# Kernel tuning notes

Measured on AMD Instinct MI355X. Metric: run time of the kernel, lower is better.

## Reference

```python
import jax, jax.numpy as jnp
import numpy as np

B, S, N, C, D = 1, 6, 6400, 128, 4
HEADS, POINTS = 4, 20
HS, WS = 32, 88
M = HS * WS
DH = C // HEADS


def setup_inputs() -> dict:
    key = jax.random.key(0)
    ks = jax.random.split(key, 16)
    sc = 0.02
    return {
        "query": jax.random.normal(ks[0], (B, N, C), jnp.float32),
        "key": jax.random.normal(ks[1], (S, M, B, C), jnp.float32),
        "value": jax.random.normal(ks[2], (S, M, B, C), jnp.float32),
        "query_pos": jax.random.normal(ks[3], (B, N, C), jnp.float32),
        "reference_points_cam": jax.random.uniform(ks[4], (S, B, N, D, 2), jnp.float32),
        "bev_mask": jax.random.bernoulli(ks[5], 0.3, (S, B, N, D)),
        "spatial_shapes": jnp.array([[HS, WS]], jnp.int32),
        "level_start_index": jnp.zeros((1,), jnp.int32),
        "Wv": sc * jax.random.normal(ks[6], (C, C), jnp.float32),
        "bv": jnp.zeros((C,), jnp.float32),
        "Woff": sc * jax.random.normal(ks[7], (C, HEADS * POINTS * 2), jnp.float32),
        "boff": sc * jax.random.normal(ks[8], (HEADS * POINTS * 2,), jnp.float32),
        "Wattn": sc * jax.random.normal(ks[9], (C, HEADS * POINTS), jnp.float32),
        "battn": jnp.zeros((HEADS * POINTS,), jnp.float32),
        "Wout": sc * jax.random.normal(ks[10], (C, C), jnp.float32),
        "bout": jnp.zeros((C,), jnp.float32),
    }


def _bilinear(img, x, y):
    # img: (G, HS, WS, DH); x, y: (G, Q, P) pixel coords (grid_sample align_corners=False, zero padding)
    G = img.shape[0]
    flat = img.reshape(G, HS * WS, DH)
    x0 = jnp.floor(x)
    y0 = jnp.floor(y)
    wx1 = x - x0
    wy1 = y - y0
    x0i = x0.astype(jnp.int32)
    y0i = y0.astype(jnp.int32)

    def gather(xi, yi):
        valid = ((xi >= 0) & (xi < WS) & (yi >= 0) & (yi < HS)).astype(img.dtype)
        idx = jnp.clip(yi, 0, HS - 1) * WS + jnp.clip(xi, 0, WS - 1)
        v = jnp.take_along_axis(flat, idx.reshape(G, -1, 1), axis=1)
        return v.reshape(*idx.shape, DH) * valid[..., None]

    v00 = gather(x0i, y0i)
    v01 = gather(x0i + 1, y0i)
    v10 = gather(x0i, y0i + 1)
    v11 = gather(x0i + 1, y0i + 1)
    return (v00 * ((1 - wx1) * (1 - wy1))[..., None]
            + v01 * (wx1 * (1 - wy1))[..., None]
            + v10 * ((1 - wx1) * wy1)[..., None]
            + v11 * (wx1 * wy1)[..., None])


def _deform_attn(q, v, ref, spatial_shapes, Wv, bv, Woff, boff, Wattn, battn):
    # q: (bs, nq, C); v: (bs, M, C); ref: (bs, nq, D, 2) in [0,1]
    bs, nq, _ = q.shape
    val = (v @ Wv + bv).reshape(bs, HS, WS, HEADS, DH)
    val = val.transpose(0, 3, 1, 2, 4).reshape(bs * HEADS, HS, WS, DH)
    # sampling offsets, normalized by (W, H), split points into POINTS//D groups per Z-anchor
    norm = jnp.stack([spatial_shapes[0, 1], spatial_shapes[0, 0]]).astype(q.dtype)  # [W, H]
    off = (q @ Woff + boff).reshape(bs, nq, HEADS, POINTS // D, D, 2) / norm
    loc = ref[:, :, None, None, :, :] + off  # (bs, nq, HEADS, P//D, D, 2)
    loc = loc.reshape(bs, nq, HEADS, POINTS, 2).transpose(0, 2, 1, 3, 4)
    loc = loc.reshape(bs * HEADS, nq, POINTS, 2)
    x = loc[..., 0] * WS - 0.5
    y = loc[..., 1] * HS - 0.5
    sampled = _bilinear(val, x, y)  # (bs*HEADS, nq, POINTS, DH)
    aw = jax.nn.softmax((q @ Wattn + battn).reshape(bs, nq, HEADS, POINTS), axis=-1)
    aw = aw.transpose(0, 2, 1, 3).reshape(bs * HEADS, nq, POINTS)
    out = jnp.einsum('gnpd,gnp->gnd', sampled, aw)
    return out.reshape(bs, HEADS, nq, DH).transpose(0, 2, 1, 3).reshape(bs, nq, C)


def reference(query, key, value, query_pos, reference_points_cam, bev_mask,
              spatial_shapes, level_start_index,
              Wv, bv, Woff, boff, Wattn, battn, Wout, bout):
    residual = query
    q = query + query_pos
    # camera routing mask (original derives indexes from batch 0 of bev_mask)
    mask0 = (bev_mask[:, 0].sum(-1) > 0).astype(q.dtype)  # (S, N)
    # dense masked equivalent of gather/pad/attend/scatter-add: deformable attn is
    # per-query independent, so computing all queries per camera and masking is exact.
    qs = jnp.broadcast_to(q[:, None], (B, S, N, C)).reshape(B * S, N, C)
    vs = value.transpose(2, 0, 1, 3).reshape(B * S, M, C)
    refs = reference_points_cam.transpose(1, 0, 2, 3, 4).reshape(B * S, N, D, 2)
    out = _deform_attn(qs, vs, refs, spatial_shapes, Wv, bv, Woff, boff, Wattn, battn)
    out = out.reshape(B, S, N, C)
    slots = (out * mask0[None, :, :, None]).sum(1)  # (B, N, C)
    count = (bev_mask.sum(-1) > 0).astype(q.dtype).transpose(1, 2, 0).sum(-1)  # (B, N)
    slots = slots / jnp.maximum(count, 1.0)[..., None]
    slots = slots @ Wout + bout
    return slots + residual  # dropout is identity in eval
```

## Files before the change

kernel.cpp:

```cpp
#include <hip/hip_runtime.h>

#define SC 6
#define NQ 6400
#define CH 128
#define HSY 32
#define WSX 88
#define MV 2816
#define NH 4
#define NP 20
#define DD 4
#define DHC 32
#define NPG 5
#define NPAIR (SC * NH * NP)

#define NB_QPROJ 800
#define NB_VPROJ 1056
#define NB_MEGA  (1 + NB_QPROJ + NB_VPROJ)

#define WS_QOFF     38464
#define WS_AW       1062464
#define WS_VAL      1574464
#define WS_SLOTS    3737152

__device__ __forceinline__ unsigned short f32_to_bf16(float x) {
    unsigned int u = __float_as_uint(x);
    unsigned int r = (u + 0x7FFFu + ((u >> 16) & 1u)) >> 16;
    return (unsigned short)r;
}

#define QB 8
__global__ __launch_bounds__(256) void k_mega(
        const unsigned int* __restrict__ bm,
        const float* __restrict__ q, const float* __restrict__ qpos,
        const float* __restrict__ Woff, const float* __restrict__ boff,
        const float* __restrict__ Wattn, const float* __restrict__ battn,
        const float* __restrict__ value, const float* __restrict__ Wv,
        const float* __restrict__ bv,
        int* __restrict__ flag, float* __restrict__ qoff,
        float* __restrict__ aw, unsigned short* __restrict__ valw) {
    __shared__ __align__(16) float smem[2048];
    int bid = blockIdx.x;
    int t = threadIdx.x;

    if (bid == 0) {
        unsigned int* r_or = (unsigned int*)smem;
        unsigned int* r_vi = r_or + 256;
        unsigned int o = 0u, v = 0u;
        for (int i = t; i < 2048; i += 256) {
            unsigned int w = bm[i];
            o |= (w & 0xFFFFFF00u);
            v |= (unsigned int)((w != 0u) & (w != 0x3F800000u));
        }
        r_or[t] = o; r_vi[t] = v;
        __syncthreads();
        for (int s = 128; s > 0; s >>= 1) {
            if (t < s) { r_or[t] |= r_or[t + s]; r_vi[t] |= r_vi[t + s]; }
            __syncthreads();
        }
        if (t == 0) {
            int f;
            if (!r_vi[0]) f = 2;
            else if (r_or[0]) f = 1;
            else f = 0;
            *flag = f;
        }
        return;
    }

    if (bid <= NB_QPROJ) {
        float (*qs)[QB] = (float(*)[QB])smem;
        float (*lg)[NH * NP] = (float(*)[NH * NP])(smem + CH * QB);
        int n0 = (bid - 1) * QB;
        for (int i = t; i < QB * CH; i += 256) {
            int qi = i >> 7, k = i & 127;
            int gi = (n0 + qi) * CH + k;
            qs[k][qi] = q[gi] + qpos[gi];
        }
        __syncthreads();
        if (t < 160) {
            float acc[QB];
#pragma unroll
            for (int qi = 0; qi < QB; ++qi) acc[qi] = 0.f;
            for (int k = 0; k < CH; ++k) {
                float w = Woff[k * 160 + t];
                float4 a = *(const float4*)&qs[k][0];
                float4 b = *(const float4*)&qs[k][4];
                acc[0] += a.x * w; acc[1] += a.y * w; acc[2] += a.z * w; acc[3] += a.w * w;
                acc[4] += b.x * w; acc[5] += b.y * w; acc[6] += b.z * w; acc[7] += b.w * w;
            }
            float b = boff[t];
#pragma unroll
            for (int qi = 0; qi < QB; ++qi) qoff[(n0 + qi) * 160 + t] = acc[qi] + b;
        } else if (t < 240) {
            int j = t - 160;
            float acc[QB];
#pragma unroll
            for (int qi = 0; qi < QB; ++qi) acc[qi] = 0.f;
            for (int k = 0; k < CH; ++k) {
                float w = Wattn[k * 80 + j];
                float4 a = *(const float4*)&qs[k][0];
                float4 b = *(const float4*)&qs[k][4];
                acc[0] += a.x * w; acc[1] += a.y * w; acc[2] += a.z * w; acc[3] += a.w * w;
                acc[4] += b.x * w; acc[5] += b.y * w; acc[6] += b.z * w; acc[7] += b.w * w;
            }
            float b = battn[j];
#pragma unroll
            for (int qi = 0; qi < QB; ++qi) lg[qi][j] = acc[qi] + b;
        }
        __syncthreads();
        if (t < QB * NH) {
            int qi = t >> 2, h = t & 3;
            float mx = -1e30f;
#pragma unroll
            for (int p = 0; p < NP; ++p) mx = fmaxf(mx, lg[qi][h * NP + p]);
            float e[NP];
            float sm = 0.f;
#pragma unroll
            for (int p = 0; p < NP; ++p) { e[p] = __expf(lg[qi][h * NP + p] - mx); sm += e[p]; }
            float inv = 1.f / sm;
#pragma unroll
            for (int p = 0; p < NP; ++p) aw[(n0 + qi) * 80 + h * NP + p] = e[p] * inv;
        }
        return;
    }

    {
        float (*vs)[16] = (float(*)[16])smem;
        int r0 = (bid - 1 - NB_QPROJ) * 16;
        for (int i = t; i < 16 * CH; i += 256) {
            int ri = i >> 7, k = i & 127;
            vs[k][ri] = value[(size_t)(r0 + ri) * CH + k];
        }
        __syncthreads();
        int c = t & 127, rh = t >> 7;
        float acc[8];
#pragma unroll
        for (int ri = 0; ri < 8; ++ri) acc[ri] = 0.f;
        for (int k = 0; k < CH; ++k) {
            float w = Wv[k * CH + c];
            float4 a = *(const float4*)&vs[k][rh * 8];
            float4 b = *(const float4*)&vs[k][rh * 8 + 4];
            acc[0] += a.x * w; acc[1] += a.y * w; acc[2] += a.z * w; acc[3] += a.w * w;
            acc[4] += b.x * w; acc[5] += b.y * w; acc[6] += b.z * w; acc[7] += b.w * w;
        }
        float b = bv[c];
        int h = c >> 5, dh = c & 31;
#pragma unroll
        for (int ri = 0; ri < 8; ++ri) {
            int r = r0 + rh * 8 + ri;
            int s = r / MV;
            int m = r - s * MV;
            valw[(size_t)((s * NH + h) * MV + m) * DHC + dh] = f32_to_bf16(acc[ri] + b);
        }
    }
}

#define REDP 36
__global__ __launch_bounds__(320) void k_sample(
        const float* __restrict__ ref, const float* __restrict__ qoff,
        const float* __restrict__ aw, const void* __restrict__ bm,
        const int* __restrict__ flag, const unsigned short* __restrict__ valw,
        float* __restrict__ slots) {
    int bid = blockIdx.x;
    int n = (bid & 7) * (NQ / 8) + (bid >> 3);
    int t = threadIdx.x;

    __shared__ float awl[NH * NP];
    __shared__ float qo[160];
    __shared__ float rf[SC][DD][2];
    __shared__ float mk[SC];
    __shared__ int   pairI[NPAIR][4];
    __shared__ float pairW[NPAIR][4];
    __shared__ float red[80][REDP];

    if (t < NH * NP) awl[t] = aw[n * 80 + t];
    if (t >= 80 && t < 240) qo[t - 80] = qoff[n * 160 + (t - 80)];
    if (t >= 240 && t < 240 + SC * DD * 2) {
        int i = t - 240;
        int s = i >> 3, rem = i & 7;
        rf[s][rem >> 1][rem & 1] = ref[(size_t)(s * NQ + n) * 8 + rem];
    }
    if (t >= 288 && t < 288 + SC) {
        int s = t - 288;
        int i = s * NQ + n;
        int f = *flag;
        int any;
        if (f == 1) {
            const unsigned char* p = (const unsigned char*)bm + (size_t)i * 4;
            any = (int)(p[0] | p[1] | p[2] | p[3]);
        } else if (f == 0) {
            const int* p = (const int*)bm + (size_t)i * 4;
            any = p[0] | p[1] | p[2] | p[3];
        } else {
            const float* p = (const float*)bm + (size_t)i * 4;
            any = (p[0] != 0.f) | (p[1] != 0.f) | (p[2] != 0.f) | (p[3] != 0.f);
        }
        mk[s] = any ? 1.0f : 0.0f;
    }
    __syncthreads();

    for (int i = t; i < NPAIR; i += 320) {
        int s = i / (NH * NP);
        int q = i - s * (NH * NP);
        int h = q & 3;
        int p = q >> 2;
        int g = p >> 2, d = p & 3;
        float x = rf[s][d][0] * (float)WSX + qo[((h * NPG + g) * DD + d) * 2 + 0] - 0.5f;
        float y = rf[s][d][1] * (float)HSY + qo[((h * NPG + g) * DD + d) * 2 + 1] - 0.5f;
        float xf = floorf(x), yf = floorf(y);
        float wx = x - xf, wy = y - yf;
        int x0 = (int)xf, y0 = (int)yf;
        int x1 = x0 + 1, y1 = y0 + 1;
        float vx0 = (x0 >= 0 && x0 < WSX) ? 1.f : 0.f;
        float vx1 = (x1 >= 0 && x1 < WSX) ? 1.f : 0.f;
        float vy0 = (y0 >= 0 && y0 < HSY) ? 1.f : 0.f;
        float vy1 = (y1 >= 0 && y1 < HSY) ? 1.f : 0.f;
        int cx0 = min(max(x0, 0), WSX - 1), cx1 = min(max(x1, 0), WSX - 1);
        int cy0 = min(max(y0, 0), HSY - 1), cy1 = min(max(y1, 0), HSY - 1);
        int base = (s * NH + h) * MV;
        pairI[i][0] = (base + cy0 * WSX + cx0) * DHC;
        pairI[i][1] = (base + cy0 * WSX + cx1) * DHC;
        pairI[i][2] = (base + cy1 * WSX + cx0) * DHC;
        pairI[i][3] = (base + cy1 * WSX + cx1) * DHC;
        float a = awl[h * NP + p];
        pairW[i][0] = (1.f - wx) * (1.f - wy) * vx0 * vy0 * a;
        pairW[i][1] = wx * (1.f - wy) * vx1 * vy0 * a;
        pairW[i][2] = (1.f - wx) * wy * vx0 * vy1 * a;
        pairW[i][3] = wx * wy * vx1 * vy1 * a;
    }
    __syncthreads();

    int sid = t >> 2;
    int c8 = t & 3;
    int coff = c8 * 8;
    float acc[8];
#pragma unroll
    for (int j = 0; j < 8; ++j) acc[j] = 0.f;
    for (int s = 0; s < SC; ++s) {
        if (mk[s] == 0.f) continue;
        int pr = s * (NH * NP) + sid;
        int4  ii = *(const int4*)pairI[pr];
        float4 ww = *(const float4*)pairW[pr];
#define CORNER(IDX, W)  {                                              \
            uint4 u = *(const uint4*)(valw + (IDX) + coff);            \
            float w_ = (W);                                            \
            acc[0] += w_ * __uint_as_float(u.x << 16);                 \
            acc[1] += w_ * __uint_as_float(u.x & 0xFFFF0000u);         \
            acc[2] += w_ * __uint_as_float(u.y << 16);                 \
            acc[3] += w_ * __uint_as_float(u.y & 0xFFFF0000u);         \
            acc[4] += w_ * __uint_as_float(u.z << 16);                 \
            acc[5] += w_ * __uint_as_float(u.z & 0xFFFF0000u);         \
            acc[6] += w_ * __uint_as_float(u.w << 16);                 \
            acc[7] += w_ * __uint_as_float(u.w & 0xFFFF0000u);         \
        }
        CORNER(ii.x, ww.x)
        CORNER(ii.y, ww.y)
        CORNER(ii.z, ww.z)
        CORNER(ii.w, ww.w)
#undef CORNER
    }
    *(float4*)&red[sid][coff] = make_float4(acc[0], acc[1], acc[2], acc[3]);
    *(float4*)&red[sid][coff + 4] = make_float4(acc[4], acc[5], acc[6], acc[7]);
    __syncthreads();

    if (t < CH) {
        int h = t >> 5, ch = t & 31;
        float sum = 0.f;
#pragma unroll
        for (int p = 0; p < NP; ++p) sum += red[p * 4 + h][ch];
        float cnt = mk[0] + mk[1] + mk[2] + mk[3] + mk[4] + mk[5];
        slots[(size_t)n * CH + t] = sum / fmaxf(cnt, 1.0f);
    }
}

__global__ void k_out(const float* __restrict__ slots, const float* __restrict__ Wout,
                      const float* __restrict__ bout, const float* __restrict__ query,
                      float* __restrict__ out) {
    __shared__ float sl[CH][QB];
    int n0 = blockIdx.x * QB;
    int t = threadIdx.x;
    for (int i = t; i < QB * CH; i += 128) {
        int qi = i >> 7, k = i & 127;
        sl[k][qi] = slots[(size_t)(n0 + qi) * CH + k];
    }
    __syncthreads();
    float acc[QB];
#pragma unroll
    for (int qi = 0; qi < QB; ++qi) acc[qi] = 0.f;
    for (int k = 0; k < CH; ++k) {
        float w = Wout[k * CH + t];
        float4 a = *(const float4*)&sl[k][0];
        float4 b = *(const float4*)&sl[k][4];
        acc[0] += a.x * w; acc[1] += a.y * w; acc[2] += a.z * w; acc[3] += a.w * w;
        acc[4] += b.x * w; acc[5] += b.y * w; acc[6] += b.z * w; acc[7] += b.w * w;
    }
    float b = bout[t];
#pragma unroll
    for (int qi = 0; qi < QB; ++qi) {
        int gi = (n0 + qi) * CH + t;
        out[gi] = acc[qi] + b + query[gi];
    }
}

extern "C" void kernel_launch(void* const* d_in, const int* in_sizes, int n_in,
                              void* d_out, int out_size, void* d_ws, size_t ws_size,
                              hipStream_t stream) {
    const float* query     = (const float*)d_in[0];
    const float* value     = (const float*)d_in[2];
    const float* query_pos = (const float*)d_in[3];
    const float* refcam    = (const float*)d_in[4];
    const void*  bev_mask  = (const void*)d_in[5];
    const float* Wv    = (const float*)d_in[8];
    const float* bv    = (const float*)d_in[9];
    const float* Woff  = (const float*)d_in[10];
    const float* boff  = (const float*)d_in[11];
    const float* Wattn = (const float*)d_in[12];
    const float* battn = (const float*)d_in[13];
    const float* Wout  = (const float*)d_in[14];
    const float* bout  = (const float*)d_in[15];

    float* wsf   = (float*)d_ws;
    int*   flag  = (int*)d_ws;
    float* qoff  = wsf + WS_QOFF;
    float* aw    = wsf + WS_AW;
    unsigned short* valw = (unsigned short*)(wsf + WS_VAL);
    float* slots = wsf + WS_SLOTS;
    float* out   = (float*)d_out;

    k_mega<<<NB_MEGA, 256, 0, stream>>>((const unsigned int*)bev_mask,
                                        query, query_pos, Woff, boff, Wattn, battn,
                                        value, Wv, bv, flag, qoff, aw, valw);
    k_sample<<<NQ, 320, 0, stream>>>(refcam, qoff, aw, bev_mask, flag, valw, slots);
    k_out<<<NQ / QB, 128, 0, stream>>>(slots, Wout, bout, query, out);
}
```

Baseline: 165.1 us.

## Fuse output projection into sampling kernel, processing two queries per block

The separate output-projection kernel is removed. Its GEMV (slots @ Wout + bias + residual) now runs at the end of the sampling kernel, and each block handles two queries in sequence. This drops a kernel launch and the round trip of the slots buffer through global memory. In exchange, every block re-reads the full 64KB Wout matrix for only two queries (reuse was eight queries per block before), the per-query phases run serially with more barriers, and the grid is halved.

Result: no change. 164.3 us (-0.5%).

```diff
diff --git a/kernel.cpp b/kernel.cpp
--- a/kernel.cpp
+++ b/kernel.cpp
@@ -20,7 +20,6 @@
 #define WS_QOFF     38464
 #define WS_AW       1062464
 #define WS_VAL      1574464
-#define WS_SLOTS    3737152
 
 __device__ __forceinline__ unsigned short f32_to_bf16(float x) {
     unsigned int u = __float_as_uint(x);
@@ -156,91 +155,103 @@
 }
 
 #define REDP 36
-__global__ __launch_bounds__(320) void k_sample(
+__global__ __launch_bounds__(320) void k_sample2(
         const float* __restrict__ ref, const float* __restrict__ qoff,
         const float* __restrict__ aw, const void* __restrict__ bm,
         const int* __restrict__ flag, const unsigned short* __restrict__ valw,
-        float* __restrict__ slots) {
+        const float* __restrict__ Wout, const float* __restrict__ bout,
+        const float* __restrict__ query, float* __restrict__ out) {
     int bid = blockIdx.x;
-    int n = (bid & 7) * (NQ / 8) + (bid >> 3);
+    int pi = (bid & 7) * (NQ / 16) + (bid >> 3);
+    int n0 = pi * 2;
     int t = threadIdx.x;
 
-    __shared__ float awl[NH * NP];
-    __shared__ float qo[160];
-    __shared__ float rf[SC][DD][2];
-    __shared__ float mk[SC];
+    __shared__ float qo[2][160];
+    __shared__ float awl[2][NH * NP];
+    __shared__ float rf[2][SC][DD][2];
+    __shared__ float mk[2][SC];
     __shared__ int   pairI[NPAIR][4];
     __shared__ float pairW[NPAIR][4];
     __shared__ float red[80][REDP];
-
-    if (t < NH * NP) awl[t] = aw[n * 80 + t];
-    if (t >= 80 && t < 240) qo[t - 80] = qoff[n * 160 + (t - 80)];
-    if (t >= 240 && t < 240 + SC * DD * 2) {
-        int i = t - 240;
-        int s = i >> 3, rem = i & 7;
-        rf[s][rem >> 1][rem & 1] = ref[(size_t)(s * NQ + n) * 8 + rem];
-    }
-    if (t >= 288 && t < 288 + SC) {
-        int s = t - 288;
-        int i = s * NQ + n;
+    __shared__ float sl[2][CH];
+
+    {
+        int qq = t / 160, idx = t - qq * 160;
+        qo[qq][idx] = qoff[(size_t)(n0 + qq) * 160 + idx];
+    }
+    if (t < 160) {
+        int qq = t / 80, idx = t - qq * 80;
+        awl[qq][idx] = aw[(size_t)(n0 + qq) * 80 + idx];
+    }
+    if (t >= 160 && t < 256) {
+        int i = t - 160;
+        int qq = i / 48, rem = i - qq * 48;
+        int s = rem >> 3, r2 = rem & 7;
+        rf[qq][s][r2 >> 1][r2 & 1] = ref[(size_t)(s * NQ + n0 + qq) * 8 + r2];
+    }
+    if (t >= 256 && t < 256 + 2 * SC) {
+        int i = t - 256;
+        int qq = i / SC, s = i - qq * SC;
+        int gi = s * NQ + n0 + qq;
         int f = *flag;
         int any;
         if (f == 1) {
-            const unsigned char* p = (const unsigned char*)bm + (size_t)i * 4;
+            const unsigned char* p = (const unsigned char*)bm + (size_t)gi * 4;
             any = (int)(p[0] | p[1] | p[2] | p[3]);
         } else if (f == 0) {
-            const int* p = (const int*)bm + (size_t)i * 4;
+            const int* p = (const int*)bm + (size_t)gi * 4;
             any = p[0] | p[1] | p[2] | p[3];
         } else {
-            const float* p = (const float*)bm + (size_t)i * 4;
+            const float* p = (const float*)bm + (size_t)gi * 4;
             any = (p[0] != 0.f) | (p[1] != 0.f) | (p[2] != 0.f) | (p[3] != 0.f);
         }
-        mk[s] = any ? 1.0f : 0.0f;
+        mk[qq][s] = any ? 1.0f : 0.0f;
     }
     __syncthreads();
 
-    for (int i = t; i < NPAIR; i += 320) {
-        int s = i / (NH * NP);
-        int q = i - s * (NH * NP);
-        int h = q & 3;
-        int p = q >> 2;
-        int g = p >> 2, d = p & 3;
-        float x = rf[s][d][0] * (float)WSX + qo[((h * NPG + g) * DD + d) * 2 + 0] - 0.5f;
-        float y = rf[s][d][1] * (float)HSY + qo[((h * NPG + g) * DD + d) * 2 + 1] - 0.5f;
-        float xf = floorf(x), yf = floorf(y);
-        float wx = x - xf, wy = y - yf;
-        int x0 = (int)xf, y0 = (int)yf;
-        int x1 = x0 + 1, y1 = y0 + 1;
-        float vx0 = (x0 >= 0 && x0 < WSX) ? 1.f : 0.f;
-        float vx1 = (x1 >= 0 && x1 < WSX) ? 1.f : 0.f;
-        float vy0 = (y0 >= 0 && y0 < HSY) ? 1.f : 0.f;
-        float vy1 = (y1 >= 0 && y1 < HSY) ? 1.f : 0.f;
-        int cx0 = min(max(x0, 0), WSX - 1), cx1 = min(max(x1, 0), WSX - 1);
-        int cy0 = min(max(y0, 0), HSY - 1), cy1 = min(max(y1, 0), HSY - 1);
-        int base = (s * NH + h) * MV;
-        pairI[i][0] = (base + cy0 * WSX + cx0) * DHC;
-        pairI[i][1] = (base + cy0 * WSX + cx1) * DHC;
-        pairI[i][2] = (base + cy1 * WSX + cx0) * DHC;
-        pairI[i][3] = (base + cy1 * WSX + cx1) * DHC;
-        float a = awl[h * NP + p];
-        pairW[i][0] = (1.f - wx) * (1.f - wy) * vx0 * vy0 * a;
-        pairW[i][1] = wx * (1.f - wy) * vx1 * vy0 * a;
-        pairW[i][2] = (1.f - wx) * wy * vx0 * vy1 * a;
-        pairW[i][3] = wx * wy * vx1 * vy1 * a;
-    }
-    __syncthreads();
-
-    int sid = t >> 2;
-    int c8 = t & 3;
-    int coff = c8 * 8;
-    float acc[8];
-#pragma unroll
-    for (int j = 0; j < 8; ++j) acc[j] = 0.f;
-    for (int s = 0; s < SC; ++s) {
-        if (mk[s] == 0.f) continue;
-        int pr = s * (NH * NP) + sid;
-        int4  ii = *(const int4*)pairI[pr];
-        float4 ww = *(const float4*)pairW[pr];
+    for (int qq = 0; qq < 2; ++qq) {
+        for (int i = t; i < NPAIR; i += 320) {
+            int s = i / (NH * NP);
+            int q = i - s * (NH * NP);
+            int h = q & 3;
+            int p = q >> 2;
+            int g = p >> 2, d = p & 3;
+            float x = rf[qq][s][d][0] * (float)WSX + qo[qq][((h * NPG + g) * DD + d) * 2 + 0] - 0.5f;
+            float y = rf[qq][s][d][1] * (float)HSY + qo[qq][((h * NPG + g) * DD + d) * 2 + 1] - 0.5f;
+            float xf = floorf(x), yf = floorf(y);
+            float wx = x - xf, wy = y - yf;
+            int x0 = (int)xf, y0 = (int)yf;
+            int x1 = x0 + 1, y1 = y0 + 1;
+            float vx0 = (x0 >= 0 && x0 < WSX) ? 1.f : 0.f;
+            float vx1 = (x1 >= 0 && x1 < WSX) ? 1.f : 0.f;
+            float vy0 = (y0 >= 0 && y0 < HSY) ? 1.f : 0.f;
+            float vy1 = (y1 >= 0 && y1 < HSY) ? 1.f : 0.f;
+            int cx0 = min(max(x0, 0), WSX - 1), cx1 = min(max(x1, 0), WSX - 1);
+            int cy0 = min(max(y0, 0), HSY - 1), cy1 = min(max(y1, 0), HSY - 1);
+            int base = (s * NH + h) * MV;
+            pairI[i][0] = (base + cy0 * WSX + cx0) * DHC;
+            pairI[i][1] = (base + cy0 * WSX + cx1) * DHC;
+            pairI[i][2] = (base + cy1 * WSX + cx0) * DHC;
+            pairI[i][3] = (base + cy1 * WSX + cx1) * DHC;
+            float a = awl[qq][h * NP + p];
+            pairW[i][0] = (1.f - wx) * (1.f - wy) * vx0 * vy0 * a;
+            pairW[i][1] = wx * (1.f - wy) * vx1 * vy0 * a;
+            pairW[i][2] = (1.f - wx) * wy * vx0 * vy1 * a;
+            pairW[i][3] = wx * wy * vx1 * vy1 * a;
+        }
+        __syncthreads();
+
+        int sid = t >> 2;
+        int c8 = t & 3;
+        int coff = c8 * 8;
+        float acc[8];
+#pragma unroll
+        for (int j = 0; j < 8; ++j) acc[j] = 0.f;
+        for (int s = 0; s < SC; ++s) {
+            if (mk[qq][s] == 0.f) continue;
+            int pr = s * (NH * NP) + sid;
+            int4  ii = *(const int4*)pairI[pr];
+            float4 ww = *(const float4*)pairW[pr];
 #define CORNER(IDX, W)  {                                              \
             uint4 u = *(const uint4*)(valw + (IDX) + coff);            \
             float w_ = (W);                                            \
@@ -253,52 +264,34 @@
             acc[6] += w_ * __uint_as_float(u.w << 16);                 \
             acc[7] += w_ * __uint_as_float(u.w & 0xFFFF0000u);         \
         }
-        CORNER(ii.x, ww.x)
-        CORNER(ii.y, ww.y)
-        CORNER(ii.z, ww.z)
-        CORNER(ii.w, ww.w)
+            CORNER(ii.x, ww.x)
+            CORNER(ii.y, ww.y)
+            CORNER(ii.z, ww.z)
+            CORNER(ii.w, ww.w)
 #undef CORNER
-    }
-    *(float4*)&red[sid][coff] = make_float4(acc[0], acc[1], acc[2], acc[3]);
-    *(float4*)&red[sid][coff + 4] = make_float4(acc[4], acc[5], acc[6], acc[7]);
-    __syncthreads();
-
-    if (t < CH) {
-        int h = t >> 5, ch = t & 31;
-        float sum = 0.f;
-#pragma unroll
-        for (int p = 0; p < NP; ++p) sum += red[p * 4 + h][ch];
-        float cnt = mk[0] + mk[1] + mk[2] + mk[3] + mk[4] + mk[5];
-        slots[(size_t)n * CH + t] = sum / fmaxf(cnt, 1.0f);
-    }
-}
-
-__global__ void k_out(const float* __restrict__ slots, const float* __restrict__ Wout,
-                      const float* __restrict__ bout, const float* __restrict__ query,
-                      float* __restrict__ out) {
-    __shared__ float sl[CH][QB];
-    int n0 = blockIdx.x * QB;
-    int t = threadIdx.x;
-    for (int i = t; i < QB * CH; i += 128) {
-        int qi = i >> 7, k = i & 127;
-        sl[k][qi] = slots[(size_t)(n0 + qi) * CH + k];
-    }
-    __syncthreads();
-    float acc[QB];
-#pragma unroll
-    for (int qi = 0; qi < QB; ++qi) acc[qi] = 0.f;
-    for (int k = 0; k < CH; ++k) {
-        float w = Wout[k * CH + t];
-        float4 a = *(const float4*)&sl[k][0];
-        float4 b = *(const float4*)&sl[k][4];
-        acc[0] += a.x * w; acc[1] += a.y * w; acc[2] += a.z * w; acc[3] += a.w * w;
-        acc[4] += b.x * w; acc[5] += b.y * w; acc[6] += b.z * w; acc[7] += b.w * w;
-    }
-    float b = bout[t];
-#pragma unroll
-    for (int qi = 0; qi < QB; ++qi) {
-        int gi = (n0 + qi) * CH + t;
-        out[gi] = acc[qi] + b + query[gi];
+        }
+        *(float4*)&red[sid][coff] = make_float4(acc[0], acc[1], acc[2], acc[3]);
+        *(float4*)&red[sid][coff + 4] = make_float4(acc[4], acc[5], acc[6], acc[7]);
+        __syncthreads();
+
+        if (t < CH) {
+            int h = t >> 5, ch = t & 31;
+            float sum = 0.f;
+#pragma unroll
+            for (int p = 0; p < NP; ++p) sum += red[p * 4 + h][ch];
+            float cnt = mk[qq][0] + mk[qq][1] + mk[qq][2] + mk[qq][3] + mk[qq][4] + mk[qq][5];
+            sl[qq][t] = sum / fmaxf(cnt, 1.0f);
+        }
+        __syncthreads();
+    }
+
+    if (t < 256) {
+        int c = t & 127;
+        int qq = t >> 7;
+        float acc = 0.f;
+        for (int k = 0; k < CH; ++k) acc += sl[qq][k] * Wout[k * CH + c];
+        int gi = (n0 + qq) * CH + c;
+        out[gi] = acc + bout[c] + query[gi];
     }
 }
 
@@ -324,12 +317,11 @@
     float* qoff  = wsf + WS_QOFF;
     float* aw    = wsf + WS_AW;
     unsigned short* valw = (unsigned short*)(wsf + WS_VAL);
-    float* slots = wsf + WS_SLOTS;
     float* out   = (float*)d_out;
 
     k_mega<<<NB_MEGA, 256, 0, stream>>>((const unsigned int*)bev_mask,
                                         query, query_pos, Woff, boff, Wattn, battn,
                                         value, Wv, bv, flag, qoff, aw, valw);
-    k_sample<<<NQ, 320, 0, stream>>>(refcam, qoff, aw, bev_mask, flag, valw, slots);
-    k_out<<<NQ / QB, 128, 0, stream>>>(slots, Wout, bout, query, out);
+    k_sample2<<<NQ / 2, 320, 0, stream>>>(refcam, qoff, aw, bev_mask, flag, valw,
+                                          Wout, bout, query, out);
 }
```
